# Kernel tuning notes

Hardware: AMD Instinct MI355X
Metric: run time of the kernel (lower is better)

The kernel has to match this reference:

```python
import jax, jax.numpy as jnp
import numpy as np

# Forest layout: 6 levels, children of node i at level L are contiguous at level L+1.
LEVEL_SIZES = [4096, 16384, 65536, 131072, 262144, 262144]
OFF = np.concatenate([[0], np.cumsum(LEVEL_SIZES)]).astype(np.int64)
N_NODES = int(OFF[-1])
VOCAB = 50000
D_IN = 128
HID = 128
N_CLASS = 4
W_SCALE = 0.08  # keep gate pre-activations in a sane range


def setup_inputs() -> dict:
    key = jax.random.key(0)
    ks = jax.random.split(key, 24)
    inp = {}
    inp["sen"] = jax.random.randint(ks[0], (N_NODES,), 0, VOCAB, dtype=jnp.int32)
    inp["embedding"] = jax.random.normal(ks[1], (VOCAB, D_IN), jnp.float32)
    names = ["ix", "ih", "fx", "fh", "ox", "oh", "ux", "uh"]
    for j, nm in enumerate(names):
        din = D_IN if nm.endswith("x") else HID
        inp["W_" + nm] = jax.random.normal(ks[2 + j], (din, HID), jnp.float32) * W_SCALE
        inp["b_" + nm] = jnp.zeros((HID,), jnp.float32)
    inp["W_out"] = jax.random.normal(ks[20], (HID, N_CLASS), jnp.float32) * W_SCALE
    inp["b_out"] = jnp.zeros((N_CLASS,), jnp.float32)
    return inp


def _forward(sen, embedding, W_ix, b_ix, W_ih, b_ih, W_fx, b_fx, W_fh, b_fh,
             W_ox, b_ox, W_oh, b_oh, W_ux, b_ux, W_uh, b_uh, W_out, b_out):
    emb = embedding[sen]                               # [N, D_in] gather
    h_all = jnp.zeros((N_NODES, HID), emb.dtype)
    c_all = jnp.zeros((N_NODES, HID), emb.dtype)
    L_last = len(LEVEL_SIZES) - 1
    for L in range(L_last, -1, -1):                    # bottom-up over levels
        o0, o1 = int(OFF[L]), int(OFF[L + 1])
        nL = LEVEL_SIZES[L]
        x = emb[o0:o1]                                 # [nL, D_in]
        if L == L_last:                                # leaves: no children
            h_sum = jnp.zeros((nL, HID), emb.dtype)
            fc_sum = jnp.zeros((nL, HID), emb.dtype)
        else:
            c0, c1 = int(OFF[L + 1]), int(OFF[L + 2])
            ratio = LEVEL_SIZES[L + 1] // nL           # children per node
            hc = h_all[c0:c1].reshape(nL, ratio, HID)  # children h
            cc = c_all[c0:c1].reshape(nL, ratio, HID)  # children c
            h_sum = hc.sum(axis=1)
            # per-child forget gate: sigmoid(fx(x_parent) + fh(h_child))
            f = jax.nn.sigmoid((x @ W_fx + b_fx)[:, None, :] + hc @ W_fh + b_fh)
            fc_sum = (f * cc).sum(axis=1)
        i = jax.nn.sigmoid(x @ W_ix + b_ix + h_sum @ W_ih + b_ih)
        og = jax.nn.sigmoid(x @ W_ox + b_ox + h_sum @ W_oh + b_oh)
        u = jnp.tanh(x @ W_ux + b_ux + h_sum @ W_uh + b_uh)
        c = i * u + fc_sum
        h = og * jnp.tanh(c)
        h_all = h_all.at[o0:o1].set(h)
        c_all = c_all.at[o0:o1].set(c)
    root_h = h_all[: LEVEL_SIZES[0]]                   # level-0 nodes
    return root_h @ W_out + b_out                      # [n_roots, 4] logits


def reference(sen, embedding, W_ix, b_ix, W_ih, b_ih, W_fx, b_fx, W_fh, b_fh,
              W_ox, b_ox, W_oh, b_oh, W_ux, b_ux, W_uh, b_uh, W_out, b_out):
    return _forward(sen, embedding, W_ix, b_ix, W_ih, b_ih, W_fx, b_fx, W_fh, b_fh,
                    W_ox, b_ox, W_oh, b_oh, W_ux, b_ux, W_uh, b_uh, W_out, b_out)
```

## Files before the change

### kernel.cpp

```cpp
#include <hip/hip_runtime.h>
#include <hip/hip_bf16.h>
#include <cstdio>

typedef unsigned short u16;
typedef __bf16 bf16x8 __attribute__((ext_vector_type(8)));
typedef float  floatx4 __attribute__((ext_vector_type(4)));

__device__ __forceinline__ float bf2f(u16 u) {
  union { unsigned int i; float f; } v; v.i = ((unsigned int)u) << 16; return v.f;
}
__device__ __forceinline__ u16 f2bf(float f) {
  union { float f; unsigned int i; } v; v.f = f;
  unsigned int x = v.i;
  return (u16)((x + 0x7fffu + ((x >> 16) & 1u)) >> 16);
}
__device__ __forceinline__ unsigned int f2bf_pk(float a, float b) {
  __hip_bfloat162 h = __float22bfloat162_rn(make_float2(a, b));
  union { __hip_bfloat162 h; unsigned int u; } v; v.h = h; return v.u;
}
__device__ __forceinline__ float sigmoidf_(float x) {
  return __builtin_amdgcn_rcpf(1.f + __expf(-x));
}
__device__ __forceinline__ float tanhf_(float x) {
  return fmaf(-2.f, __builtin_amdgcn_rcpf(1.f + __expf(2.f * x)), 1.f);
}

__device__ __forceinline__ int swz128(int row, int c16) {
  return row * 128 + ((c16 ^ (row & 15)) << 3);
}
__device__ __forceinline__ int swze(int row, int col) {
  return row * 128 + (((((col >> 3)) ^ (row & 15)) << 3) | (col & 7));
}

__global__ __launch_bounds__(256, 2) void proj_e(
    const float* __restrict__ emb, const u16* __restrict__ WT,
    const float* __restrict__ bsum, u16* __restrict__ Ep)
{
  __shared__ __align__(16) u16 ldsA[128 * 128];
  const int tid = threadIdx.x;
  const long m0 = (long)blockIdx.x * 128;
  {
    const int r = tid >> 1, half = tid & 1;
    long row = m0 + r; if (row > 49999) row = 49999;
    const float* src = emb + row * 128 + half * 64;
#pragma unroll
    for (int i = 0; i < 8; i++) {
      float4 v0 = *reinterpret_cast<const float4*>(src + i * 8);
      float4 v1 = *reinterpret_cast<const float4*>(src + i * 8 + 4);
      unsigned int ov[4] = { f2bf_pk(v0.x, v0.y), f2bf_pk(v0.z, v0.w),
                             f2bf_pk(v1.x, v1.y), f2bf_pk(v1.z, v1.w) };
      *reinterpret_cast<uint4*>(&ldsA[swz128(r, half * 8 + i)]) =
          *reinterpret_cast<const uint4*>(ov);
    }
  }
  __syncthreads();
  const int lane = tid & 63, w = tid >> 6, l16 = lane & 15, quad = lane >> 4;
#pragma unroll
  for (int half = 0; half < 2; half++) {
    const int col = w * 32 + half * 16 + l16;
    bf16x8 bI[4], bU[4], bO[4], bF[4];
#pragma unroll
    for (int ks = 0; ks < 4; ks++) {
      const size_t o_ = ks * 32 + quad * 8;
      bI[ks] = *reinterpret_cast<const bf16x8*>(WT + (size_t)(0   + col) * 128 + o_);
      bU[ks] = *reinterpret_cast<const bf16x8*>(WT + (size_t)(128 + col) * 128 + o_);
      bO[ks] = *reinterpret_cast<const bf16x8*>(WT + (size_t)(256 + col) * 128 + o_);
      bF[ks] = *reinterpret_cast<const bf16x8*>(WT + (size_t)(384 + col) * 128 + o_);
    }
    const float bi = bsum[col], bu = bsum[128 + col], bo = bsum[256 + col], bf = bsum[384 + col];
#pragma unroll
    for (int i = 0; i < 8; i++) {
      floatx4 aI = {0.f,0.f,0.f,0.f}, aU = {0.f,0.f,0.f,0.f};
      floatx4 aO = {0.f,0.f,0.f,0.f}, aF = {0.f,0.f,0.f,0.f};
#pragma unroll
      for (int ks = 0; ks < 4; ks++) {
        bf16x8 a = *reinterpret_cast<const bf16x8*>(&ldsA[swz128(i * 16 + l16, ks * 4 + quad)]);
        aI = __builtin_amdgcn_mfma_f32_16x16x32_bf16(a, bI[ks], aI, 0, 0, 0);
        aU = __builtin_amdgcn_mfma_f32_16x16x32_bf16(a, bU[ks], aU, 0, 0, 0);
        aO = __builtin_amdgcn_mfma_f32_16x16x32_bf16(a, bO[ks], aO, 0, 0, 0);
        aF = __builtin_amdgcn_mfma_f32_16x16x32_bf16(a, bF[ks], aF, 0, 0, 0);
      }
#pragma unroll
      for (int r2 = 0; r2 < 4; r2++) {
        const long row = m0 + i * 16 + quad * 4 + r2;
        if (row < 50000) {
          u16 ov[4] = { f2bf(aI[r2] + bi), f2bf(aU[r2] + bu),
                        f2bf(aO[r2] + bo), f2bf(aF[r2] + bf) };
          *reinterpret_cast<ushort4*>(Ep + row * 512 + col * 4) =
              *reinterpret_cast<const ushort4*>(ov);
        }
      }
    }
  }
}

__global__ void embf(const float* __restrict__ emb, u16* __restrict__ Xb)
{
  const long idx = (long)blockIdx.x * 256 + threadIdx.x;
  float4 v = *reinterpret_cast<const float4*>(emb + idx * 4);
  unsigned int o[2] = { f2bf_pk(v.x, v.y), f2bf_pk(v.z, v.w) };
  *reinterpret_cast<uint2*>(Xb + idx * 4) = *reinterpret_cast<const uint2*>(o);
}

__global__ void leaf_hc(const u16* __restrict__ Ep,
                        u16* __restrict__ Hl, u16* __restrict__ Cl)
{
  const int tid = threadIdx.x;
  const int r = tid >> 6, c2 = tid & 63;
  const size_t v = (size_t)blockIdx.x * 4 + r;
  uint4 g = *reinterpret_cast<const uint4*>(Ep + v * 512 + (size_t)c2 * 8);
  const u16* p = reinterpret_cast<const u16*>(&g);
  float c0 = sigmoidf_(bf2f(p[0])) * tanhf_(bf2f(p[1]));
  float c1 = sigmoidf_(bf2f(p[4])) * tanhf_(bf2f(p[5]));
  float h0 = sigmoidf_(bf2f(p[2])) * tanhf_(c0);
  float h1 = sigmoidf_(bf2f(p[6])) * tanhf_(c1);
  *reinterpret_cast<unsigned int*>(Hl + v * 128 + c2 * 2) = f2bf_pk(h0, h1);
  *reinterpret_cast<unsigned int*>(Cl + v * 128 + c2 * 2) = f2bf_pk(c0, c1);
}

__global__ __launch_bounds__(256, 2) void k_l3fused(
    const int* __restrict__ sen, const u16* __restrict__ Ep,
    const u16* __restrict__ Xb, const u16* __restrict__ Hl, const u16* __restrict__ Cl,
    const u16* __restrict__ WxT, const float* __restrict__ bsum,
    const u16* __restrict__ BfT, const u16* __restrict__ BihT,
    const u16* __restrict__ BuhT, const u16* __restrict__ BohT,
    u16* __restrict__ c_out, u16* __restrict__ h_out,
    long o0, long o1, long o2)
{
  constexpr int PM = 32, CM = 64, NCI = 4, RT = 2;
  __shared__ __align__(16) u16 ldsX[CM * 128];
  __shared__ __align__(16) u16 ldsH[CM * 128];
  __shared__ __align__(16) u16 ldsC[CM * 128];
  __shared__ __align__(16) u16 ldsA[CM * 128];
  __shared__ int sidP[PM];

  const int tid = threadIdx.x;
  const long p0 = (long)blockIdx.x * PM;
  const long cb = (long)blockIdx.x * CM;

  {
    const int r = tid >> 2, q = tid & 3;
    const size_t vp = (size_t)sen[o1 + cb + r];
    const size_t vc = (size_t)sen[o2 + cb + r];
    const u16* xb = Xb + vp * 128;
    const u16* hl = Hl + vc * 128;
    const u16* cl = Cl + vc * 128;
#pragma unroll
    for (int ii = 0; ii < 4; ii++) {
      const int c16 = q * 4 + ii;
      *reinterpret_cast<uint4*>(&ldsX[swz128(r, c16)]) =
          *reinterpret_cast<const uint4*>(xb + c16 * 8);
      *reinterpret_cast<uint4*>(&ldsH[swz128(r, c16)]) =
          *reinterpret_cast<const uint4*>(hl + c16 * 8);
      *reinterpret_cast<uint4*>(&ldsC[swz128(r, c16)]) =
          *reinterpret_cast<const uint4*>(cl + c16 * 8);
    }
    if (tid < PM) sidP[tid] = sen[o0 + p0 + tid];
  }
  __syncthreads();

  const int lane = tid & 63, w = tid >> 6, l16 = lane & 15, quad = lane >> 4;

#pragma unroll
  for (int gl = 0; gl < 2; gl++) {
    const int col = w * 32 + gl * 16 + l16;
    bf16x8 xI[4], xU[4], xO[4], xF[4], hI[4], hU[4], hO[4], hF[4];
#pragma unroll
    for (int ks = 0; ks < 4; ks++) {
      const size_t xo = ks * 32 + quad * 8;
      xI[ks] = *reinterpret_cast<const bf16x8*>(WxT + (size_t)(0   + col) * 128 + xo);
      xU[ks] = *reinterpret_cast<const bf16x8*>(WxT + (size_t)(128 + col) * 128 + xo);
      xO[ks] = *reinterpret_cast<const bf16x8*>(WxT + (size_t)(256 + col) * 128 + xo);
      xF[ks] = *reinterpret_cast<const bf16x8*>(WxT + (size_t)(384 + col) * 128 + xo);
      const size_t ho = (size_t)col * 128 + xo;
      hI[ks] = *reinterpret_cast<const bf16x8*>(BihT + ho);
      hU[ks] = *reinterpret_cast<const bf16x8*>(BuhT + ho);
      hO[ks] = *reinterpret_cast<const bf16x8*>(BohT + ho);
      hF[ks] = *reinterpret_cast<const bf16x8*>(BfT  + ho);
    }
    const float bi = bsum[col], bu = bsum[128 + col], bo = bsum[256 + col], bf = bsum[384 + col];
#pragma unroll
    for (int i = 0; i < NCI; i++) {
      floatx4 aI = {0.f,0.f,0.f,0.f}, aU = {0.f,0.f,0.f,0.f};
      floatx4 aO = {0.f,0.f,0.f,0.f}, aF = {0.f,0.f,0.f,0.f};
#pragma unroll
      for (int ks = 0; ks < 4; ks++) {
        bf16x8 ax = *reinterpret_cast<const bf16x8*>(&ldsX[swz128(i * 16 + l16, ks * 4 + quad)]);
        aI = __builtin_amdgcn_mfma_f32_16x16x32_bf16(ax, xI[ks], aI, 0, 0, 0);
        aU = __builtin_amdgcn_mfma_f32_16x16x32_bf16(ax, xU[ks], aU, 0, 0, 0);
        aO = __builtin_amdgcn_mfma_f32_16x16x32_bf16(ax, xO[ks], aO, 0, 0, 0);
        aF = __builtin_amdgcn_mfma_f32_16x16x32_bf16(ax, xF[ks], aF, 0, 0, 0);
      }
#pragma unroll
      for (int ks = 0; ks < 4; ks++) {
        bf16x8 ah = *reinterpret_cast<const bf16x8*>(&ldsH[swz128(i * 16 + l16, ks * 4 + quad)]);
        aI = __builtin_amdgcn_mfma_f32_16x16x32_bf16(ah, hI[ks], aI, 0, 0, 0);
        aU = __builtin_amdgcn_mfma_f32_16x16x32_bf16(ah, hU[ks], aU, 0, 0, 0);
        aO = __builtin_amdgcn_mfma_f32_16x16x32_bf16(ah, hO[ks], aO, 0, 0, 0);
        aF = __builtin_amdgcn_mfma_f32_16x16x32_bf16(ah, hF[ks], aF, 0, 0, 0);
      }
      const int rbase = i * 16 + quad * 4;
#pragma unroll
      for (int r2 = 0; r2 < 4; r2++) {
        const int row = rbase + r2;
        const float iv = sigmoidf_(aI[r2] + bi);
        const float uv = tanhf_   (aU[r2] + bu);
        const float ov = sigmoidf_(aO[r2] + bo);
        const float fv = sigmoidf_(aF[r2] + bf);
        const int sl = swze(row, col);
        const float clv = bf2f(ldsC[sl]);
        const float c4 = fmaf(iv, uv, fv * clv);
        const float h4 = ov * tanhf_(c4);
        ldsC[sl] = f2bf(c4);
        ldsA[sl] = f2bf(h4);
      }
    }
  }
  __syncthreads();

#pragma unroll
  for (int gl = 0; gl < 2; gl++) {
    const int col = w * 32 + gl * 16 + l16;
    bf16x8 bF[4], bI[4], bU[4], bO[4];
#pragma unroll
    for (int ks = 0; ks < 4; ks++) {
      const size_t bo_ = (size_t)col * 128 + ks * 32 + quad * 8;
      bF[ks] = *reinterpret_cast<const bf16x8*>(BfT + bo_);
      bI[ks] = *reinterpret_cast<const bf16x8*>(BihT + bo_);
      bU[ks] = *reinterpret_cast<const bf16x8*>(BuhT + bo_);
      bO[ks] = *reinterpret_cast<const bf16x8*>(BohT + bo_);
    }
#pragma unroll
    for (int i = 0; i < NCI; i++) {
      floatx4 aF = {0.f,0.f,0.f,0.f}, aI = {0.f,0.f,0.f,0.f};
      floatx4 aU = {0.f,0.f,0.f,0.f}, aO = {0.f,0.f,0.f,0.f};
#pragma unroll
      for (int ks = 0; ks < 4; ks++) {
        bf16x8 a = *reinterpret_cast<const bf16x8*>(&ldsA[swz128(i * 16 + l16, ks * 4 + quad)]);
        aF = __builtin_amdgcn_mfma_f32_16x16x32_bf16(a, bF[ks], aF, 0, 0, 0);
        aI = __builtin_amdgcn_mfma_f32_16x16x32_bf16(a, bI[ks], aI, 0, 0, 0);
        aU = __builtin_amdgcn_mfma_f32_16x16x32_bf16(a, bU[ks], aU, 0, 0, 0);
        aO = __builtin_amdgcn_mfma_f32_16x16x32_bf16(a, bO[ks], aO, 0, 0, 0);
      }
      const int rbase = i * 16 + quad * 4;
#pragma unroll
      for (int t = 0; t < 2; t++) {
        const int p = (rbase >> 1) + t;
        ushort4 g4 = *reinterpret_cast<const ushort4*>(Ep + (size_t)sidP[p] * 512 + col * 4);
        const float epf = bf2f(g4.w);
        float fsum = 0.f, isum = 0.f, usum = 0.f, osum = 0.f;
#pragma unroll
        for (int r2 = t * RT; r2 < t * RT + RT; r2++) {
          const int row = rbase + r2;
          const float cch = bf2f(ldsC[swze(row, col)]);
          fsum += sigmoidf_(aF[r2] + epf) * cch;
          isum += aI[r2]; usum += aU[r2]; osum += aO[r2];
        }
        const float c = sigmoidf_(isum + bf2f(g4.x)) * tanhf_(usum + bf2f(g4.y)) + fsum;
        const float h = sigmoidf_(osum + bf2f(g4.z)) * tanhf_(c);
        c_out[(p0 + p) * 128 + col] = f2bf(c);
        h_out[(p0 + p) * 128 + col] = f2bf(h);
      }
    }
  }
}

template<int LR>
__global__ __launch_bounds__(256, 2) void k_level(
    const int* __restrict__ sen, const u16* __restrict__ Ep,
    const u16* __restrict__ h_prev, const u16* __restrict__ c_prev,
    const u16* __restrict__ BfT, const u16* __restrict__ BihT,
    const u16* __restrict__ BuhT, const u16* __restrict__ BohT,
    u16* __restrict__ c_out, u16* __restrict__ h_out,
    long o0)
{
  constexpr int PM  = (LR == 2) ? 32 : 64;
  constexpr int CM  = PM << LR;
  constexpr int NCI = CM / 16;
  constexpr int RT  = 1 << LR;
  constexpr int RTI = 4 >> LR;
  constexpr int TPR = 256 / CM;
  __shared__ __align__(16) u16 ldsA[CM * 128];
  __shared__ int sidP[PM];

  const int tid = threadIdx.x;
  const long p0 = (long)blockIdx.x * PM;
  const long cb = (long)blockIdx.x * CM;

  {
    const int r = tid / TPR, q = tid % TPR;
    constexpr int CH = 16 / TPR;
    const u16* src = h_prev + (cb + r) * 128;
#pragma unroll
    for (int ii = 0; ii < CH; ii++) {
      const int c16 = q * CH + ii;
      *reinterpret_cast<uint4*>(&ldsA[swz128(r, c16)]) =
          *reinterpret_cast<const uint4*>(src + c16 * 8);
    }
    if (tid < PM) sidP[tid] = sen[o0 + p0 + tid];
  }
  __syncthreads();

  const int lane = tid & 63, w = tid >> 6, l16 = lane & 15, quad = lane >> 4;

#pragma unroll
  for (int gl = 0; gl < 2; gl++) {
    const int col = w * 32 + gl * 16 + l16;
    bf16x8 bF[4], bI[4], bU[4], bO[4];
#pragma unroll
    for (int ks = 0; ks < 4; ks++) {
      const size_t bo_ = (size_t)col * 128 + ks * 32 + quad * 8;
      bF[ks] = *reinterpret_cast<const bf16x8*>(BfT + bo_);
      bI[ks] = *reinterpret_cast<const bf16x8*>(BihT + bo_);
      bU[ks] = *reinterpret_cast<const bf16x8*>(BuhT + bo_);
      bO[ks] = *reinterpret_cast<const bf16x8*>(BohT + bo_);
    }
#pragma unroll
    for (int i = 0; i < NCI; i++) {
      floatx4 aF = {0.f,0.f,0.f,0.f}, aI = {0.f,0.f,0.f,0.f};
      floatx4 aU = {0.f,0.f,0.f,0.f}, aO = {0.f,0.f,0.f,0.f};
#pragma unroll
      for (int ks = 0; ks < 4; ks++) {
        bf16x8 a = *reinterpret_cast<const bf16x8*>(&ldsA[swz128(i * 16 + l16, ks * 4 + quad)]);
        aF = __builtin_amdgcn_mfma_f32_16x16x32_bf16(a, bF[ks], aF, 0, 0, 0);
        aI = __builtin_amdgcn_mfma_f32_16x16x32_bf16(a, bI[ks], aI, 0, 0, 0);
        aU = __builtin_amdgcn_mfma_f32_16x16x32_bf16(a, bU[ks], aU, 0, 0, 0);
        aO = __builtin_amdgcn_mfma_f32_16x16x32_bf16(a, bO[ks], aO, 0, 0, 0);
      }
      const int rbase = i * 16 + quad * 4;
#pragma unroll
      for (int t = 0; t < RTI; t++) {
        const int p = (rbase >> LR) + t;
        ushort4 g4 = *reinterpret_cast<const ushort4*>(Ep + (size_t)sidP[p] * 512 + col * 4);
        const float epf = bf2f(g4.w);
        float fsum = 0.f, isum = 0.f, usum = 0.f, osum = 0.f;
#pragma unroll
        for (int r2 = t * RT; r2 < t * RT + RT; r2++) {
          const int row = rbase + r2;
          const float cch = bf2f(c_prev[(cb + row) * 128 + col]);
          fsum += sigmoidf_(aF[r2] + epf) * cch;
          isum += aI[r2]; usum += aU[r2]; osum += aO[r2];
        }
        const float c = sigmoidf_(isum + bf2f(g4.x)) * tanhf_(usum + bf2f(g4.y)) + fsum;
        const float h = sigmoidf_(osum + bf2f(g4.z)) * tanhf_(c);
        c_out[(p0 + p) * 128 + col] = f2bf(c);
        h_out[(p0 + p) * 128 + col] = f2bf(h);
      }
    }
  }
}

__global__ void build_wallT(const float* __restrict__ Wix, const float* __restrict__ Wux,
                            const float* __restrict__ Wox, const float* __restrict__ Wfx,
                            u16* __restrict__ WT)
{
  int idx = blockIdx.x * 256 + threadIdx.x;
  int n = idx >> 7, k = idx & 127;
  int g = n >> 7, j = n & 127;
  const float* W = (g == 0) ? Wix : (g == 1) ? Wux : (g == 2) ? Wox : Wfx;
  WT[idx] = f2bf(W[k * 128 + j]);
}

__global__ void build_bsum(const float* __restrict__ b_ix, const float* __restrict__ b_ih,
                           const float* __restrict__ b_ux, const float* __restrict__ b_uh,
                           const float* __restrict__ b_ox, const float* __restrict__ b_oh,
                           const float* __restrict__ b_fx, const float* __restrict__ b_fh,
                           float* __restrict__ bsum)
{
  int n = blockIdx.x * 256 + threadIdx.x;
  int g = n >> 7, j = n & 127;
  float v = (g == 0) ? b_ix[j] + b_ih[j] : (g == 1) ? b_ux[j] + b_uh[j]
          : (g == 2) ? b_ox[j] + b_oh[j] : b_fx[j] + b_fh[j];
  bsum[n] = v;
}

__global__ void build_bt128(const float* __restrict__ W, u16* __restrict__ BT) {
  int idx = blockIdx.x * 256 + threadIdx.x;
  int n = idx >> 7, k = idx & 127;
  BT[idx] = f2bf(W[k * 128 + n]);
}

__global__ void out_proj(const u16* __restrict__ h_root, const float* __restrict__ W_out,
                         const float* __restrict__ b_out, float* __restrict__ out)
{
  int idx = blockIdx.x * 256 + threadIdx.x;
  int n = idx >> 2, cls = idx & 3;
  float s = b_out[cls];
  for (int k = 0; k < 128; k++)
    s += bf2f(h_root[(long)n * 128 + k]) * W_out[k * 4 + cls];
  out[idx] = s;
}

extern "C" void kernel_launch(void* const* d_in, const int* in_sizes, int n_in,
                              void* d_out, int out_size, void* d_ws, size_t ws_size,
                              hipStream_t stream)
{
  const int*   sen  = (const int*)d_in[0];
  const float* emb  = (const float*)d_in[1];
  const float* W_ix = (const float*)d_in[2];  const float* b_ix = (const float*)d_in[3];
  const float* W_ih = (const float*)d_in[4];  const float* b_ih = (const float*)d_in[5];
  const float* W_fx = (const float*)d_in[6];  const float* b_fx = (const float*)d_in[7];
  const float* W_fh = (const float*)d_in[8];  const float* b_fh = (const float*)d_in[9];
  const float* W_ox = (const float*)d_in[10]; const float* b_ox = (const float*)d_in[11];
  const float* W_oh = (const float*)d_in[12]; const float* b_oh = (const float*)d_in[13];
  const float* W_ux = (const float*)d_in[14]; const float* b_ux = (const float*)d_in[15];
  const float* W_uh = (const float*)d_in[16]; const float* b_uh = (const float*)d_in[17];
  const float* W_out= (const float*)d_in[18]; const float* b_out= (const float*)d_in[19];
  float* out = (float*)d_out;

  const size_t EPB = (size_t)50000 * 512 * 2;
  const size_t TBB = (size_t)50000 * 128 * 2;
  const size_t H3  = (size_t)131072 * 128 * 2;
  const size_t H2  = (size_t)65536  * 128 * 2;
  const size_t H1  = (size_t)16384  * 128 * 2;
  const size_t H0  = (size_t)4096   * 128 * 2;
  const size_t need = EPB + 3 * TBB + 2 * (H3 + H2 + H1 + H0)
                    + (size_t)512 * 128 * 2 + 4 * (size_t)128 * 128 * 2 + 512 * 4 + 8192;
  fprintf(stderr, "[tree_lstm] ws_size=%zu need=%zu\n", ws_size, need);
  if (ws_size < need) {
    fprintf(stderr, "[tree_lstm] INSUFFICIENT WORKSPACE — skipping launch\n");
    return;
  }
  char* ws = (char*)d_ws;
  size_t off = 0;
  auto take = [&](size_t bytes) { char* p = ws + off; off += (bytes + 255) & ~(size_t)255; return p; };
  u16* Ep = (u16*)take(EPB);
  u16* Xb = (u16*)take(TBB);
  u16* Hl = (u16*)take(TBB);
  u16* Cl = (u16*)take(TBB);
  u16* h3 = (u16*)take(H3);  u16* c3 = (u16*)take(H3);
  u16* h2 = (u16*)take(H2);  u16* c2 = (u16*)take(H2);
  u16* h1 = (u16*)take(H1);  u16* c1 = (u16*)take(H1);
  u16* h0 = (u16*)take(H0);  u16* c0 = (u16*)take(H0);
  u16* WallT = (u16*)take((size_t)512 * 128 * 2);
  u16* BihT = (u16*)take((size_t)128 * 128 * 2);
  u16* BuhT = (u16*)take((size_t)128 * 128 * 2);
  u16* BohT = (u16*)take((size_t)128 * 128 * 2);
  u16* BfhT = (u16*)take((size_t)128 * 128 * 2);
  float* bsum = (float*)take(512 * 4);

  build_wallT<<<256, 256, 0, stream>>>(W_ix, W_ux, W_ox, W_fx, WallT);
  build_bsum<<<2, 256, 0, stream>>>(b_ix, b_ih, b_ux, b_uh, b_ox, b_oh, b_fx, b_fh, bsum);
  build_bt128<<<64, 256, 0, stream>>>(W_ih, BihT);
  build_bt128<<<64, 256, 0, stream>>>(W_uh, BuhT);
  build_bt128<<<64, 256, 0, stream>>>(W_oh, BohT);
  build_bt128<<<64, 256, 0, stream>>>(W_fh, BfhT);
  proj_e<<<391, 256, 0, stream>>>(emb, WallT, bsum, Ep);
  embf<<<6250, 256, 0, stream>>>(emb, Xb);
  leaf_hc<<<12500, 256, 0, stream>>>(Ep, Hl, Cl);

  const long LOFF[6] = {0, 4096, 20480, 86016, 217088, 479232};

  k_l3fused<<<4096, 256, 0, stream>>>(sen, Ep, Xb, Hl, Cl, WallT, bsum,
      BfhT, BihT, BuhT, BohT, c3, h3, LOFF[3], LOFF[4], LOFF[5]);
  k_level<1><<<1024, 256, 0, stream>>>(sen, Ep, h3, c3,
      BfhT, BihT, BuhT, BohT, c2, h2, LOFF[2]);
  k_level<2><<<512, 256, 0, stream>>>(sen, Ep, h2, c2,
      BfhT, BihT, BuhT, BohT, c1, h1, LOFF[1]);
  k_level<2><<<128, 256, 0, stream>>>(sen, Ep, h1, c1,
      BfhT, BihT, BuhT, BohT, c0, h0, LOFF[0]);

  out_proj<<<64, 256, 0, stream>>>(h0, W_out, b_out, out);
}
```

Before: 536.6 us.

## Use precomputed vocab projections in fused level-3 kernel instead of recomputing x@Wx

```diff
diff --git a/kernel.cpp b/kernel.cpp
--- a/kernel.cpp
+++ b/kernel.cpp
@@ -92,14 +92,6 @@
       }
     }
   }
-}
-
-__global__ void embf(const float* __restrict__ emb, u16* __restrict__ Xb)
-{
-  const long idx = (long)blockIdx.x * 256 + threadIdx.x;
-  float4 v = *reinterpret_cast<const float4*>(emb + idx * 4);
-  unsigned int o[2] = { f2bf_pk(v.x, v.y), f2bf_pk(v.z, v.w) };
-  *reinterpret_cast<uint2*>(Xb + idx * 4) = *reinterpret_cast<const uint2*>(o);
 }
 
 __global__ void leaf_hc(const u16* __restrict__ Ep,
@@ -120,18 +112,17 @@
 
 __global__ __launch_bounds__(256, 2) void k_l3fused(
     const int* __restrict__ sen, const u16* __restrict__ Ep,
-    const u16* __restrict__ Xb, const u16* __restrict__ Hl, const u16* __restrict__ Cl,
-    const u16* __restrict__ WxT, const float* __restrict__ bsum,
+    const u16* __restrict__ Hl, const u16* __restrict__ Cl,
     const u16* __restrict__ BfT, const u16* __restrict__ BihT,
     const u16* __restrict__ BuhT, const u16* __restrict__ BohT,
     u16* __restrict__ c_out, u16* __restrict__ h_out,
     long o0, long o1, long o2)
 {
   constexpr int PM = 32, CM = 64, NCI = 4, RT = 2;
-  __shared__ __align__(16) u16 ldsX[CM * 128];
   __shared__ __align__(16) u16 ldsH[CM * 128];
   __shared__ __align__(16) u16 ldsC[CM * 128];
   __shared__ __align__(16) u16 ldsA[CM * 128];
+  __shared__ int sidC[CM];
   __shared__ int sidP[PM];
 
   const int tid = threadIdx.x;
@@ -139,22 +130,26 @@
   const long cb = (long)blockIdx.x * CM;
 
   {
-    const int r = tid >> 2, q = tid & 3;
-    const size_t vp = (size_t)sen[o1 + cb + r];
+    const int r = (tid & 127) >> 1, half = tid & 1;
     const size_t vc = (size_t)sen[o2 + cb + r];
-    const u16* xb = Xb + vp * 128;
-    const u16* hl = Hl + vc * 128;
-    const u16* cl = Cl + vc * 128;
-#pragma unroll
-    for (int ii = 0; ii < 4; ii++) {
-      const int c16 = q * 4 + ii;
-      *reinterpret_cast<uint4*>(&ldsX[swz128(r, c16)]) =
-          *reinterpret_cast<const uint4*>(xb + c16 * 8);
-      *reinterpret_cast<uint4*>(&ldsH[swz128(r, c16)]) =
-          *reinterpret_cast<const uint4*>(hl + c16 * 8);
-      *reinterpret_cast<uint4*>(&ldsC[swz128(r, c16)]) =
-          *reinterpret_cast<const uint4*>(cl + c16 * 8);
-    }
+    if (tid < 128) {
+      const u16* hs = Hl + vc * 128;
+#pragma unroll
+      for (int ii = 0; ii < 8; ii++) {
+        const int c16 = half * 8 + ii;
+        *reinterpret_cast<uint4*>(&ldsH[swz128(r, c16)]) =
+            *reinterpret_cast<const uint4*>(hs + c16 * 8);
+      }
+    } else {
+      const u16* cs = Cl + vc * 128;
+#pragma unroll
+      for (int ii = 0; ii < 8; ii++) {
+        const int c16 = half * 8 + ii;
+        *reinterpret_cast<uint4*>(&ldsC[swz128(r, c16)]) =
+            *reinterpret_cast<const uint4*>(cs + c16 * 8);
+      }
+    }
+    if (tid < CM) sidC[tid] = sen[o1 + cb + tid];
     if (tid < PM) sidP[tid] = sen[o0 + p0 + tid];
   }
   __syncthreads();
@@ -164,33 +159,19 @@
 #pragma unroll
   for (int gl = 0; gl < 2; gl++) {
     const int col = w * 32 + gl * 16 + l16;
-    bf16x8 xI[4], xU[4], xO[4], xF[4], hI[4], hU[4], hO[4], hF[4];
+    bf16x8 hI[4], hU[4], hO[4], hF[4];
 #pragma unroll
     for (int ks = 0; ks < 4; ks++) {
-      const size_t xo = ks * 32 + quad * 8;
-      xI[ks] = *reinterpret_cast<const bf16x8*>(WxT + (size_t)(0   + col) * 128 + xo);
-      xU[ks] = *reinterpret_cast<const bf16x8*>(WxT + (size_t)(128 + col) * 128 + xo);
-      xO[ks] = *reinterpret_cast<const bf16x8*>(WxT + (size_t)(256 + col) * 128 + xo);
-      xF[ks] = *reinterpret_cast<const bf16x8*>(WxT + (size_t)(384 + col) * 128 + xo);
-      const size_t ho = (size_t)col * 128 + xo;
+      const size_t ho = (size_t)col * 128 + ks * 32 + quad * 8;
       hI[ks] = *reinterpret_cast<const bf16x8*>(BihT + ho);
       hU[ks] = *reinterpret_cast<const bf16x8*>(BuhT + ho);
       hO[ks] = *reinterpret_cast<const bf16x8*>(BohT + ho);
       hF[ks] = *reinterpret_cast<const bf16x8*>(BfT  + ho);
     }
-    const float bi = bsum[col], bu = bsum[128 + col], bo = bsum[256 + col], bf = bsum[384 + col];
 #pragma unroll
     for (int i = 0; i < NCI; i++) {
       floatx4 aI = {0.f,0.f,0.f,0.f}, aU = {0.f,0.f,0.f,0.f};
       floatx4 aO = {0.f,0.f,0.f,0.f}, aF = {0.f,0.f,0.f,0.f};
-#pragma unroll
-      for (int ks = 0; ks < 4; ks++) {
-        bf16x8 ax = *reinterpret_cast<const bf16x8*>(&ldsX[swz128(i * 16 + l16, ks * 4 + quad)]);
-        aI = __builtin_amdgcn_mfma_f32_16x16x32_bf16(ax, xI[ks], aI, 0, 0, 0);
-        aU = __builtin_amdgcn_mfma_f32_16x16x32_bf16(ax, xU[ks], aU, 0, 0, 0);
-        aO = __builtin_amdgcn_mfma_f32_16x16x32_bf16(ax, xO[ks], aO, 0, 0, 0);
-        aF = __builtin_amdgcn_mfma_f32_16x16x32_bf16(ax, xF[ks], aF, 0, 0, 0);
-      }
 #pragma unroll
       for (int ks = 0; ks < 4; ks++) {
         bf16x8 ah = *reinterpret_cast<const bf16x8*>(&ldsH[swz128(i * 16 + l16, ks * 4 + quad)]);
@@ -203,13 +184,14 @@
 #pragma unroll
       for (int r2 = 0; r2 < 4; r2++) {
         const int row = rbase + r2;
-        const float iv = sigmoidf_(aI[r2] + bi);
-        const float uv = tanhf_   (aU[r2] + bu);
-        const float ov = sigmoidf_(aO[r2] + bo);
-        const float fv = sigmoidf_(aF[r2] + bf);
+        ushort4 e4 = *reinterpret_cast<const ushort4*>(
+            Ep + (size_t)sidC[row] * 512 + col * 4);
+        const float iv = sigmoidf_(aI[r2] + bf2f(e4.x));
+        const float uv = tanhf_   (aU[r2] + bf2f(e4.y));
+        const float ov = sigmoidf_(aO[r2] + bf2f(e4.z));
+        const float fv = sigmoidf_(aF[r2] + bf2f(e4.w));
         const int sl = swze(row, col);
-        const float clv = bf2f(ldsC[sl]);
-        const float c4 = fmaf(iv, uv, fv * clv);
+        const float c4 = fmaf(iv, uv, fv * bf2f(ldsC[sl]));
         const float h4 = ov * tanhf_(c4);
         ldsC[sl] = f2bf(c4);
         ldsA[sl] = f2bf(h4);
@@ -414,7 +396,7 @@
   const size_t H2  = (size_t)65536  * 128 * 2;
   const size_t H1  = (size_t)16384  * 128 * 2;
   const size_t H0  = (size_t)4096   * 128 * 2;
-  const size_t need = EPB + 3 * TBB + 2 * (H3 + H2 + H1 + H0)
+  const size_t need = EPB + 2 * TBB + 2 * (H3 + H2 + H1 + H0)
                     + (size_t)512 * 128 * 2 + 4 * (size_t)128 * 128 * 2 + 512 * 4 + 8192;
   fprintf(stderr, "[tree_lstm] ws_size=%zu need=%zu\n", ws_size, need);
   if (ws_size < need) {
@@ -425,7 +407,6 @@
   size_t off = 0;
   auto take = [&](size_t bytes) { char* p = ws + off; off += (bytes + 255) & ~(size_t)255; return p; };
   u16* Ep = (u16*)take(EPB);
-  u16* Xb = (u16*)take(TBB);
   u16* Hl = (u16*)take(TBB);
   u16* Cl = (u16*)take(TBB);
   u16* h3 = (u16*)take(H3);  u16* c3 = (u16*)take(H3);
@@ -446,12 +427,11 @@
   build_bt128<<<64, 256, 0, stream>>>(W_oh, BohT);
   build_bt128<<<64, 256, 0, stream>>>(W_fh, BfhT);
   proj_e<<<391, 256, 0, stream>>>(emb, WallT, bsum, Ep);
-  embf<<<6250, 256, 0, stream>>>(emb, Xb);
   leaf_hc<<<12500, 256, 0, stream>>>(Ep, Hl, Cl);
 
   const long LOFF[6] = {0, 4096, 20480, 86016, 217088, 479232};
 
-  k_l3fused<<<4096, 256, 0, stream>>>(sen, Ep, Xb, Hl, Cl, WallT, bsum,
+  k_l3fused<<<4096, 256, 0, stream>>>(sen, Ep, Hl, Cl,
       BfhT, BihT, BuhT, BohT, c3, h3, LOFF[3], LOFF[4], LOFF[5]);
   k_level<1><<<1024, 256, 0, stream>>>(sen, Ep, h3, c3,
       BfhT, BihT, BuhT, BohT, c2, h2, LOFF[2]);
```

After: 521.8 us. 2.8% less time.
